# Performance work log

Hardware: AMD Instinct MI355X
Metric: run time of the kernel (lower is better)

The kernel has to match this reference:

```python
import jax, jax.numpy as jnp
import numpy as np

N_NODES = 100000
N_EDGES = 1600000
SIZE = 64


def setup_inputs() -> dict:
    key = jax.random.key(0)
    ks = jax.random.split(key, 10)
    source = jax.random.normal(ks[0], (N_NODES, SIZE), dtype=jnp.float32)
    target = jax.random.normal(ks[1], (N_NODES, SIZE), dtype=jnp.float32)
    src_idx = jax.random.randint(ks[2], (N_EDGES,), 0, N_NODES, dtype=jnp.int64)
    seg_ids = jnp.sort(jax.random.randint(ks[3], (N_EDGES,), 0, N_NODES, dtype=jnp.int64))
    # parameters of nn.Linear(size,size) and two nn.Linear(size,1)
    s = 1.0 / np.sqrt(SIZE)
    W_emb = jax.random.uniform(ks[4], (SIZE, SIZE), jnp.float32, -s, s)
    b_emb = jax.random.uniform(ks[5], (SIZE,), jnp.float32, -s, s)
    w_loc = jax.random.uniform(ks[6], (SIZE,), jnp.float32, -s, s)
    b_loc = jax.random.uniform(ks[7], (), jnp.float32, -s, s)
    w_nb = jax.random.uniform(ks[8], (SIZE,), jnp.float32, -s, s)
    b_nb = jax.random.uniform(ks[9], (), jnp.float32, -s, s)
    return {"source": source, "target": target, "src_idx": src_idx, "seg_ids": seg_ids,
            "W_emb": W_emb, "b_emb": b_emb, "w_loc": w_loc, "b_loc": b_loc,
            "w_nb": w_nb, "b_nb": b_nb}


def reference(source, target, src_idx, seg_ids, W_emb, b_emb, w_loc, b_loc, w_nb, b_nb):
    n = target.shape[0]
    # attention_local(embedding(own_data)) per destination node -> [N]
    a_t = (target @ W_emb.T + b_emb) @ w_loc + b_loc
    # gather neighbour messages along edge list -> [E, size]
    msg = source[src_idx]
    # attention_neighbour(embedding(source_message)) per edge -> [E]
    a_s = (msg @ W_emb.T + b_emb) @ w_nb + b_nb
    scores = (a_t[seg_ids] + a_s)[:, None]  # [E, 1]
    # faithful to torch: softmax over dim=1 of [n, 1] scores (trivially ones)
    attn = jax.nn.softmax(scores, axis=1)
    # weighted sum over each node's neighbourhood -> [N, size]
    return jax.ops.segment_sum(attn * msg, seg_ids, num_segments=n)
```

## Files before the change

kernel.cpp:

```cpp
#include <hip/hip_runtime.h>


#define SIZE 64
#define WAVES_PER_BLOCK 4
#define BLOCK_THREADS (WAVES_PER_BLOCK * 64)

__global__ __launch_bounds__(256)
void build_row_starts(const int* __restrict__ seg_ids,
                      int* __restrict__ row_start,
                      int n_nodes, int n_edges) {
    int e = blockIdx.x * 256 + threadIdx.x;
    if (e >= n_edges) return;
    const int c = seg_ids[e];
    if (e == 0) {
        for (int n = 0; n <= c; ++n) row_start[n] = 0;
    } else {
        const int p = seg_ids[e - 1];
        for (int n = p + 1; n <= c; ++n) row_start[n] = e;
    }
    if (e == n_edges - 1) {
        for (int n = c + 1; n <= n_nodes; ++n) row_start[n] = n_edges;
    }
}

__global__ __launch_bounds__(BLOCK_THREADS)
void seg_sum_gather(const float* __restrict__ source,
                    const int* __restrict__ src_idx,
                    const int* __restrict__ row_start,
                    float* __restrict__ out,
                    int n_nodes) {
    int n = __builtin_amdgcn_readfirstlane(
        (int)(blockIdx.x * WAVES_PER_BLOCK + (threadIdx.x >> 6)));
    if (n >= n_nodes) return;
    const int lane = threadIdx.x & 63;

    const int start = row_start[n];
    const int end   = row_start[n + 1];

    float s0 = 0.f, s1 = 0.f, s2 = 0.f, s3 = 0.f;
    float s4 = 0.f, s5 = 0.f, s6 = 0.f, s7 = 0.f;
    int e = start;
    for (; e + 8 <= end; e += 8) {
        int i0 = src_idx[e + 0];
        int i1 = src_idx[e + 1];
        int i2 = src_idx[e + 2];
        int i3 = src_idx[e + 3];
        int i4 = src_idx[e + 4];
        int i5 = src_idx[e + 5];
        int i6 = src_idx[e + 6];
        int i7 = src_idx[e + 7];
        s0 += source[(size_t)i0 * SIZE + lane];
        s1 += source[(size_t)i1 * SIZE + lane];
        s2 += source[(size_t)i2 * SIZE + lane];
        s3 += source[(size_t)i3 * SIZE + lane];
        s4 += source[(size_t)i4 * SIZE + lane];
        s5 += source[(size_t)i5 * SIZE + lane];
        s6 += source[(size_t)i6 * SIZE + lane];
        s7 += source[(size_t)i7 * SIZE + lane];
    }
    for (; e + 2 <= end; e += 2) {
        int i0 = src_idx[e + 0];
        int i1 = src_idx[e + 1];
        s0 += source[(size_t)i0 * SIZE + lane];
        s1 += source[(size_t)i1 * SIZE + lane];
    }
    if (e < end) {
        int i0 = src_idx[e];
        s0 += source[(size_t)i0 * SIZE + lane];
    }
    const float sum = ((s0 + s1) + (s2 + s3)) + ((s4 + s5) + (s6 + s7));

    __builtin_nontemporal_store(sum, &out[(size_t)n * SIZE + lane]);
}

__global__ __launch_bounds__(BLOCK_THREADS)
void seg_sum_bsearch(const float* __restrict__ source,
                     const int* __restrict__ src_idx,
                     const int* __restrict__ seg_ids,
                     float* __restrict__ out,
                     int n_nodes, int n_edges) {
    int n = __builtin_amdgcn_readfirstlane(
        (int)(blockIdx.x * WAVES_PER_BLOCK + (threadIdx.x >> 6)));
    if (n >= n_nodes) return;
    const int lane = threadIdx.x & 63;

    int lo = 0, hi = n_edges;
    while (lo < hi) {
        int mid = (lo + hi) >> 1;
        if (seg_ids[mid] < n) lo = mid + 1; else hi = mid;
    }
    const int start = lo;
    hi = n_edges;
    while (lo < hi) {
        int mid = (lo + hi) >> 1;
        if (seg_ids[mid] < n + 1) lo = mid + 1; else hi = mid;
    }
    const int end = lo;

    float s0 = 0.f, s1 = 0.f, s2 = 0.f, s3 = 0.f;
    int e = start;
    for (; e + 4 <= end; e += 4) {
        int i0 = src_idx[e + 0];
        int i1 = src_idx[e + 1];
        int i2 = src_idx[e + 2];
        int i3 = src_idx[e + 3];
        s0 += source[(size_t)i0 * SIZE + lane];
        s1 += source[(size_t)i1 * SIZE + lane];
        s2 += source[(size_t)i2 * SIZE + lane];
        s3 += source[(size_t)i3 * SIZE + lane];
    }
    for (; e < end; ++e) {
        int i = src_idx[e];
        s0 += source[(size_t)i * SIZE + lane];
    }
    out[(size_t)n * SIZE + lane] = (s0 + s1) + (s2 + s3);
}

extern "C" void kernel_launch(void* const* d_in, const int* in_sizes, int n_in,
                              void* d_out, int out_size, void* d_ws, size_t ws_size,
                              hipStream_t stream) {
    const float* source = (const float*)d_in[0];
    const int* src_idx = (const int*)d_in[2];
    const int* seg_ids = (const int*)d_in[3];
    float* out = (float*)d_out;

    const int n_nodes = in_sizes[0] / SIZE;
    const int n_edges = in_sizes[2];

    const int grid = (n_nodes + WAVES_PER_BLOCK - 1) / WAVES_PER_BLOCK;

    const size_t need = (size_t)(n_nodes + 1) * sizeof(int);
    if (ws_size >= need && d_ws != nullptr) {
        int* row_start = (int*)d_ws;
        const int gridA = (n_edges + 255) / 256;
        build_row_starts<<<gridA, 256, 0, stream>>>(seg_ids, row_start,
                                                    n_nodes, n_edges);
        seg_sum_gather<<<grid, BLOCK_THREADS, 0, stream>>>(
            source, src_idx, row_start, out, n_nodes);
    } else {
        seg_sum_bsearch<<<grid, BLOCK_THREADS, 0, stream>>>(
            source, src_idx, seg_ids, out, n_nodes, n_edges);
    }
}
```

Baseline: 159.7 us.

## Gather neighbour rows from an fp16 copy of source with 4 edges per wave

Adds a pre-pass that converts the source feature table to fp16 in workspace. A new gather kernel then has each 16-lane quarter of a wave fetch a different edge's row with 8-byte loads, accumulate in fp32, and combine quarters via cross-lane shuffles. This halves the bytes moved per gathered row and issues fewer load instructions per edge, but adds a full conversion pass over source and introduces fp16 rounding error into the sums.

```diff
diff --git a/kernel.cpp b/kernel.cpp
--- a/kernel.cpp
+++ b/kernel.cpp
@@ -1,9 +1,14 @@
 #include <hip/hip_runtime.h>
+#include <hip/hip_fp16.h>
 
 
 #define SIZE 64
 #define WAVES_PER_BLOCK 4
 #define BLOCK_THREADS (WAVES_PER_BLOCK * 64)
+
+typedef float  f32x4 __attribute__((ext_vector_type(4)));
+typedef float  f32x2 __attribute__((ext_vector_type(2)));
+typedef unsigned int u32x2 __attribute__((ext_vector_type(2)));
 
 __global__ __launch_bounds__(256)
 void build_row_starts(const int* __restrict__ seg_ids,
@@ -20,6 +25,93 @@
     }
     if (e == n_edges - 1) {
         for (int n = c + 1; n <= n_nodes; ++n) row_start[n] = n_edges;
+    }
+}
+
+__global__ __launch_bounds__(256)
+void convert_f32_to_f16(const float* __restrict__ src,
+                        __half* __restrict__ dst, int n4) {
+    int t = blockIdx.x * 256 + threadIdx.x;
+    if (t >= n4) return;
+    const f32x4 v = ((const f32x4*)src)[t];
+    const __half2 lo = __floats2half2_rn(v.x, v.y);
+    const __half2 hi = __floats2half2_rn(v.z, v.w);
+    u32x2 o;
+    o.x = __builtin_bit_cast(unsigned int, lo);
+    o.y = __builtin_bit_cast(unsigned int, hi);
+    ((u32x2*)dst)[t] = o;
+}
+
+__global__ __launch_bounds__(BLOCK_THREADS)
+void seg_sum_gather_f16(const __half* __restrict__ src16,
+                        const int* __restrict__ src_idx,
+                        const int* __restrict__ row_start,
+                        float* __restrict__ out, int n_nodes) {
+    int n = __builtin_amdgcn_readfirstlane(
+        (int)(blockIdx.x * WAVES_PER_BLOCK + (threadIdx.x >> 6)));
+    if (n >= n_nodes) return;
+    const int lane = threadIdx.x & 63;
+    const int g = lane >> 4;
+    const int q = lane & 15;
+
+    const int start = row_start[n];
+    const int end   = row_start[n + 1];
+
+    f32x4 acc = {0.f, 0.f, 0.f, 0.f};
+    const __half* base = src16 + (size_t)q * 4;
+
+    int e = start;
+    for (; e + 16 <= end; e += 16) {
+#pragma unroll
+        for (int k = 0; k < 4; ++k) {
+            const int i0 = src_idx[e + 4 * k + 0];
+            const int i1 = src_idx[e + 4 * k + 1];
+            const int i2 = src_idx[e + 4 * k + 2];
+            const int i3 = src_idx[e + 4 * k + 3];
+            const int i = (g == 0) ? i0 : (g == 1) ? i1 : (g == 2) ? i2 : i3;
+            const u32x2 hv = *(const u32x2*)(base + (size_t)i * SIZE);
+            const unsigned int w0 = hv.x, w1 = hv.y;
+            const float2 f0 = __half22float2(__builtin_bit_cast(__half2, w0));
+            const float2 f1 = __half22float2(__builtin_bit_cast(__half2, w1));
+            acc.x += f0.x; acc.y += f0.y; acc.z += f1.x; acc.w += f1.y;
+        }
+    }
+    for (; e + 4 <= end; e += 4) {
+        const int i0 = src_idx[e + 0];
+        const int i1 = src_idx[e + 1];
+        const int i2 = src_idx[e + 2];
+        const int i3 = src_idx[e + 3];
+        const int i = (g == 0) ? i0 : (g == 1) ? i1 : (g == 2) ? i2 : i3;
+        const u32x2 hv = *(const u32x2*)(base + (size_t)i * SIZE);
+        const unsigned int w0 = hv.x, w1 = hv.y;
+        const float2 f0 = __half22float2(__builtin_bit_cast(__half2, w0));
+        const float2 f1 = __half22float2(__builtin_bit_cast(__half2, w1));
+        acc.x += f0.x; acc.y += f0.y; acc.z += f1.x; acc.w += f1.y;
+    }
+    const int rem = end - e;
+    if (rem > 0) {
+        const int i = src_idx[e + ((g < rem) ? g : 0)];
+        const u32x2 hv = *(const u32x2*)(base + (size_t)i * SIZE);
+        const unsigned int w0 = hv.x, w1 = hv.y;
+        const float2 f0 = __half22float2(__builtin_bit_cast(__half2, w0));
+        const float2 f1 = __half22float2(__builtin_bit_cast(__half2, w1));
+        const float m = (g < rem) ? 1.f : 0.f;
+        acc.x += m * f0.x; acc.y += m * f0.y;
+        acc.z += m * f1.x; acc.w += m * f1.y;
+    }
+
+    acc.x += __shfl_xor(acc.x, 32, 64);
+    acc.y += __shfl_xor(acc.y, 32, 64);
+    acc.z += __shfl_xor(acc.z, 32, 64);
+    acc.w += __shfl_xor(acc.w, 32, 64);
+    acc.x += __shfl_xor(acc.x, 16, 64);
+    acc.y += __shfl_xor(acc.y, 16, 64);
+    acc.z += __shfl_xor(acc.z, 16, 64);
+    acc.w += __shfl_xor(acc.w, 16, 64);
+
+    if (lane < 16) {
+        __builtin_nontemporal_store(
+            acc, (f32x4*)(out + (size_t)n * SIZE + (size_t)q * 4));
     }
 }
 
@@ -65,11 +157,10 @@
         s1 += source[(size_t)i1 * SIZE + lane];
     }
     if (e < end) {
-        int i0 = src_idx[e];
-        s0 += source[(size_t)i0 * SIZE + lane];
+        int i = src_idx[e];
+        s0 += source[(size_t)i * SIZE + lane];
     }
     const float sum = ((s0 + s1) + (s2 + s3)) + ((s4 + s5) + (s6 + s7));
-
     __builtin_nontemporal_store(sum, &out[(size_t)n * SIZE + lane]);
 }
 
@@ -129,8 +220,22 @@
 
     const int grid = (n_nodes + WAVES_PER_BLOCK - 1) / WAVES_PER_BLOCK;
 
-    const size_t need = (size_t)(n_nodes + 1) * sizeof(int);
-    if (ws_size >= need && d_ws != nullptr) {
+    const size_t rs_bytes = (size_t)(n_nodes + 1) * sizeof(int);
+    const size_t rs_pad   = (rs_bytes + 255) & ~(size_t)255;
+    const size_t f16_bytes = (size_t)n_nodes * SIZE * sizeof(__half);
+
+    if (d_ws != nullptr && ws_size >= rs_pad + f16_bytes) {
+        int*    row_start = (int*)d_ws;
+        __half* src16     = (__half*)((char*)d_ws + rs_pad);
+        const int gridA = (n_edges + 255) / 256;
+        build_row_starts<<<gridA, 256, 0, stream>>>(seg_ids, row_start,
+                                                    n_nodes, n_edges);
+        const int n4    = n_nodes * (SIZE / 4);
+        const int gridC = (n4 + 255) / 256;
+        convert_f32_to_f16<<<gridC, 256, 0, stream>>>(source, src16, n4);
+        seg_sum_gather_f16<<<grid, BLOCK_THREADS, 0, stream>>>(
+            src16, src_idx, row_start, out, n_nodes);
+    } else if (d_ws != nullptr && ws_size >= rs_bytes) {
         int* row_start = (int*)d_ws;
         const int gridA = (n_edges + 255) / 256;
         build_row_starts<<<gridA, 256, 0, stream>>>(seg_ids, row_start,
```

New measurement: 153.4 us, median of 2. 1.04x faster.

## Gather from fp16 feature-class-split copy of source in segment sum

Applied to the files above, without the earlier changes.

Adds a pre-pass that converts source rows to fp16 and splits each row into four 16-feature classes stored contiguously per class. The gather kernel then handles one class per block, with eight edges processed in parallel per wave (8 lanes per edge, one half2 per lane), followed by a shuffle reduction. The aim is to halve the bytes gathered and make each class's table small enough to stay in cache. The costs are an extra conversion pass, precision lost by rounding inputs to fp16, and src_idx being read four times.

```diff
diff --git a/kernel.cpp b/kernel.cpp
--- a/kernel.cpp
+++ b/kernel.cpp
@@ -1,9 +1,21 @@
 #include <hip/hip_runtime.h>
+#include <hip/hip_fp16.h>
 
 
 #define SIZE 64
 #define WAVES_PER_BLOCK 4
 #define BLOCK_THREADS (WAVES_PER_BLOCK * 64)
+#define NCLS 4
+#define CFEAT 16
+#define CPAIRS 8
+
+typedef float f32x4 __attribute__((ext_vector_type(4)));
+typedef float f32x2 __attribute__((ext_vector_type(2)));
+
+static __device__ __forceinline__ unsigned pack2(float a, float b) {
+    __half2 h = __floats2half2_rn(a, b);
+    return __builtin_bit_cast(unsigned, h);
+}
 
 __global__ __launch_bounds__(256)
 void build_row_starts(const int* __restrict__ seg_ids,
@@ -23,6 +35,61 @@
     }
 }
 
+__global__ __launch_bounds__(256)
+void convert_cls(const float* __restrict__ src,
+                 unsigned* __restrict__ dst, int n_nodes) {
+    int t = blockIdx.x * 256 + threadIdx.x;
+    if (t >= n_nodes * 32) return;
+    const int n = t >> 5;
+    const int p = t & 31;
+    const int c = p >> 3;
+    const int j = p & 7;
+    const float2 v = *(const float2*)(src + (size_t)n * SIZE + p * 2);
+    dst[((size_t)c * n_nodes + n) * CPAIRS + j] = pack2(v.x, v.y);
+}
+
+__global__ __launch_bounds__(BLOCK_THREADS)
+void seg_sum_gather_cls(const unsigned* __restrict__ srcT,
+                        const int* __restrict__ src_idx,
+                        const int* __restrict__ row_start,
+                        float* __restrict__ out, int n_nodes) {
+    const int cls  = blockIdx.x & (NCLS - 1);
+    const int nb   = blockIdx.x >> 2;
+    const int wid  = threadIdx.x >> 6;
+    const int lane = threadIdx.x & 63;
+    const int es   = lane >> 3;
+    const int sub  = lane & 7;
+
+    const int n = nb * WAVES_PER_BLOCK + wid;
+    if (n >= n_nodes) return;
+
+    const unsigned* cbase = srcT + (size_t)cls * n_nodes * CPAIRS + sub;
+    const int s = row_start[n];
+    const int t = row_start[n + 1];
+
+    float ax = 0.f, ay = 0.f;
+    for (int e = s; e < t; e += 8) {
+        const int cnt = t - e;
+        const int off = (es < cnt) ? es : 0;
+        const int i   = src_idx[e + off];
+        const unsigned w = cbase[(size_t)i * CPAIRS];
+        const float2 f = __half22float2(__builtin_bit_cast(__half2, w));
+        const float m = (es < cnt) ? 1.f : 0.f;
+        ax += m * f.x;
+        ay += m * f.y;
+    }
+#pragma unroll
+    for (int o = 8; o < 64; o <<= 1) {
+        ax += __shfl_xor(ax, o, 64);
+        ay += __shfl_xor(ay, o, 64);
+    }
+    if (lane < 8) {
+        f32x2 r; r.x = ax; r.y = ay;
+        __builtin_nontemporal_store(
+            r, (f32x2*)(out + (size_t)n * SIZE + cls * CFEAT + sub * 2));
+    }
+}
+
 __global__ __launch_bounds__(BLOCK_THREADS)
 void seg_sum_gather(const float* __restrict__ source,
                     const int* __restrict__ src_idx,
@@ -33,22 +100,16 @@
         (int)(blockIdx.x * WAVES_PER_BLOCK + (threadIdx.x >> 6)));
     if (n >= n_nodes) return;
     const int lane = threadIdx.x & 63;
-
     const int start = row_start[n];
     const int end   = row_start[n + 1];
-
     float s0 = 0.f, s1 = 0.f, s2 = 0.f, s3 = 0.f;
     float s4 = 0.f, s5 = 0.f, s6 = 0.f, s7 = 0.f;
     int e = start;
     for (; e + 8 <= end; e += 8) {
-        int i0 = src_idx[e + 0];
-        int i1 = src_idx[e + 1];
-        int i2 = src_idx[e + 2];
-        int i3 = src_idx[e + 3];
-        int i4 = src_idx[e + 4];
-        int i5 = src_idx[e + 5];
-        int i6 = src_idx[e + 6];
-        int i7 = src_idx[e + 7];
+        int i0 = src_idx[e + 0]; int i1 = src_idx[e + 1];
+        int i2 = src_idx[e + 2]; int i3 = src_idx[e + 3];
+        int i4 = src_idx[e + 4]; int i5 = src_idx[e + 5];
+        int i6 = src_idx[e + 6]; int i7 = src_idx[e + 7];
         s0 += source[(size_t)i0 * SIZE + lane];
         s1 += source[(size_t)i1 * SIZE + lane];
         s2 += source[(size_t)i2 * SIZE + lane];
@@ -58,18 +119,8 @@
         s6 += source[(size_t)i6 * SIZE + lane];
         s7 += source[(size_t)i7 * SIZE + lane];
     }
-    for (; e + 2 <= end; e += 2) {
-        int i0 = src_idx[e + 0];
-        int i1 = src_idx[e + 1];
-        s0 += source[(size_t)i0 * SIZE + lane];
-        s1 += source[(size_t)i1 * SIZE + lane];
-    }
-    if (e < end) {
-        int i0 = src_idx[e];
-        s0 += source[(size_t)i0 * SIZE + lane];
-    }
+    for (; e < end; ++e) s0 += source[(size_t)src_idx[e] * SIZE + lane];
     const float sum = ((s0 + s1) + (s2 + s3)) + ((s4 + s5) + (s6 + s7));
-
     __builtin_nontemporal_store(sum, &out[(size_t)n * SIZE + lane]);
 }
 
@@ -83,36 +134,25 @@
         (int)(blockIdx.x * WAVES_PER_BLOCK + (threadIdx.x >> 6)));
     if (n >= n_nodes) return;
     const int lane = threadIdx.x & 63;
-
     int lo = 0, hi = n_edges;
-    while (lo < hi) {
-        int mid = (lo + hi) >> 1;
-        if (seg_ids[mid] < n) lo = mid + 1; else hi = mid;
-    }
+    while (lo < hi) { int mid = (lo + hi) >> 1;
+        if (seg_ids[mid] < n) lo = mid + 1; else hi = mid; }
     const int start = lo;
     hi = n_edges;
-    while (lo < hi) {
-        int mid = (lo + hi) >> 1;
-        if (seg_ids[mid] < n + 1) lo = mid + 1; else hi = mid;
-    }
+    while (lo < hi) { int mid = (lo + hi) >> 1;
+        if (seg_ids[mid] < n + 1) lo = mid + 1; else hi = mid; }
     const int end = lo;
-
     float s0 = 0.f, s1 = 0.f, s2 = 0.f, s3 = 0.f;
     int e = start;
     for (; e + 4 <= end; e += 4) {
-        int i0 = src_idx[e + 0];
-        int i1 = src_idx[e + 1];
-        int i2 = src_idx[e + 2];
-        int i3 = src_idx[e + 3];
+        int i0 = src_idx[e + 0]; int i1 = src_idx[e + 1];
+        int i2 = src_idx[e + 2]; int i3 = src_idx[e + 3];
         s0 += source[(size_t)i0 * SIZE + lane];
         s1 += source[(size_t)i1 * SIZE + lane];
         s2 += source[(size_t)i2 * SIZE + lane];
         s3 += source[(size_t)i3 * SIZE + lane];
     }
-    for (; e < end; ++e) {
-        int i = src_idx[e];
-        s0 += source[(size_t)i * SIZE + lane];
-    }
+    for (; e < end; ++e) s0 += source[(size_t)src_idx[e] * SIZE + lane];
     out[(size_t)n * SIZE + lane] = (s0 + s1) + (s2 + s3);
 }
 
@@ -127,17 +167,34 @@
     const int n_nodes = in_sizes[0] / SIZE;
     const int n_edges = in_sizes[2];
 
-    const int grid = (n_nodes + WAVES_PER_BLOCK - 1) / WAVES_PER_BLOCK;
-
-    const size_t need = (size_t)(n_nodes + 1) * sizeof(int);
-    if (ws_size >= need && d_ws != nullptr) {
+    const size_t rs_bytes  = (size_t)(n_nodes + 1) * sizeof(int);
+    const size_t rs_pad    = (rs_bytes + 255) & ~(size_t)255;
+    const size_t f16_bytes = (size_t)NCLS * n_nodes * CPAIRS * sizeof(unsigned);
+
+    if (d_ws != nullptr && ws_size >= rs_pad + f16_bytes) {
+        int*      row_start = (int*)d_ws;
+        unsigned* srcT      = (unsigned*)((char*)d_ws + rs_pad);
+
+        const int gridA = (n_edges + 255) / 256;
+        build_row_starts<<<gridA, 256, 0, stream>>>(seg_ids, row_start,
+                                                    n_nodes, n_edges);
+        const int gridC = (n_nodes * 32 + 255) / 256;
+        convert_cls<<<gridC, 256, 0, stream>>>(source, srcT, n_nodes);
+
+        const int nb    = (n_nodes + WAVES_PER_BLOCK - 1) / WAVES_PER_BLOCK;
+        const int gridB = nb * NCLS;
+        seg_sum_gather_cls<<<gridB, BLOCK_THREADS, 0, stream>>>(
+            srcT, src_idx, row_start, out, n_nodes);
+    } else if (d_ws != nullptr && ws_size >= rs_bytes) {
         int* row_start = (int*)d_ws;
         const int gridA = (n_edges + 255) / 256;
         build_row_starts<<<gridA, 256, 0, stream>>>(seg_ids, row_start,
                                                     n_nodes, n_edges);
+        const int grid = (n_nodes + WAVES_PER_BLOCK - 1) / WAVES_PER_BLOCK;
         seg_sum_gather<<<grid, BLOCK_THREADS, 0, stream>>>(
             source, src_idx, row_start, out, n_nodes);
     } else {
+        const int grid = (n_nodes + WAVES_PER_BLOCK - 1) / WAVES_PER_BLOCK;
         seg_sum_bsearch<<<grid, BLOCK_THREADS, 0, stream>>>(
             source, src_idx, seg_ids, out, n_nodes, n_edges);
     }
```

Measured after the change: 219.0 us. 37.2% more time.
